# Kernel tuning notes

Hardware: AMD Instinct MI355X
Metric: run time of the kernel (lower is better)

The kernel has to match this reference:

```python
import jax, jax.numpy as jnp
import numpy as np

N_HEADS = 12
EMBED_DIM = 768
QKV_DIM = 64


def setup_inputs() -> dict:
    key = jax.random.key(0)
    ks = jax.random.split(key, 6)
    x = jax.random.normal(ks[0], (32, 577, EMBED_DIM), dtype=jnp.float32)
    # per-head Linear weights, torch layout [out, in] stacked over heads: [H, D, E]
    s = 1.0 / np.sqrt(EMBED_DIM)
    wq = jax.random.uniform(ks[1], (N_HEADS, QKV_DIM, EMBED_DIM), jnp.float32, -s, s)
    wk = jax.random.uniform(ks[2], (N_HEADS, QKV_DIM, EMBED_DIM), jnp.float32, -s, s)
    wv = jax.random.uniform(ks[3], (N_HEADS, QKV_DIM, EMBED_DIM), jnp.float32, -s, s)
    sp = 1.0 / np.sqrt(N_HEADS * QKV_DIM)
    w_proj = jax.random.uniform(ks[4], (EMBED_DIM, N_HEADS * QKV_DIM), jnp.float32, -sp, sp)
    b_proj = jax.random.uniform(ks[5], (EMBED_DIM,), jnp.float32, -sp, sp)
    return {"x": x, "wq": wq, "wk": wk, "wv": wv, "w_proj": w_proj, "b_proj": b_proj}


def reference(x, wq, wk, wv, w_proj, b_proj):
    scale = QKV_DIM ** (-0.5)
    # batched per-head projections: x [B,S,E], w* [H,D,E] -> [B,H,S,D]
    q = jnp.einsum('bse,hde->bhsd', x, wq)
    k = jnp.einsum('bse,hde->bhsd', x, wk)
    v = jnp.einsum('bse,hde->bhsd', x, wv)
    scores = jnp.einsum('bhsd,bhtd->bhst', q, k) * scale  # [B,H,S,S]
    attn = jax.nn.softmax(scores, axis=-1)
    out = jnp.einsum('bhst,bhtd->bhsd', attn, v)          # [B,H,S,D]
    # concat heads in head order along last dim: [B,S,H*D]
    B, H, S, D = out.shape
    cat = jnp.transpose(out, (0, 2, 1, 3)).reshape(B, S, H * D)
    return cat @ w_proj.T + b_proj
```

## Files before the change

kernel.cpp:

```cpp
#include <hip/hip_runtime.h>

#define TOK    18464
#define SEQ    577
#define EMB    768
#define NH     12
#define HD     64
#define HEADSZ 36928
#define PLANE  14180352
#define SPAD   640

typedef float f32x4 __attribute__((ext_vector_type(4)));
typedef short s16x8 __attribute__((ext_vector_type(8)));

__device__ __forceinline__ unsigned short f2bf(float f) {
  unsigned u = __builtin_bit_cast(unsigned, f);
  return (unsigned short)((u + 0x7fffu + ((u >> 16) & 1u)) >> 16);
}
__device__ __forceinline__ unsigned pk2bf(float a, float b) {
  return (unsigned)f2bf(a) | ((unsigned)f2bf(b) << 16);
}
__device__ __forceinline__ float fexp2(float x) {
  float r; asm("v_exp_f32 %0, %1" : "=v"(r) : "v"(x)); return r;
}

__device__ __forceinline__ void gload16(const void* g, void* l) {
  __builtin_amdgcn_global_load_lds(
      (const __attribute__((address_space(1))) void*)g,
      (__attribute__((address_space(3))) void*)l, 16, 0, 0);
}

__global__ void cvt_x(const float* __restrict__ src, short* __restrict__ dst, int n8) {
  int i = blockIdx.x * blockDim.x + threadIdx.x;
  if (i >= n8) return;
  const float4* s4 = reinterpret_cast<const float4*>(src + (size_t)i * 8);
  float4 a = s4[0], b = s4[1];
  s16x8 o;
  o[0] = (short)f2bf(a.x); o[1] = (short)f2bf(a.y);
  o[2] = (short)f2bf(a.z); o[3] = (short)f2bf(a.w);
  o[4] = (short)f2bf(b.x); o[5] = (short)f2bf(b.y);
  o[6] = (short)f2bf(b.z); o[7] = (short)f2bf(b.w);
  *reinterpret_cast<s16x8*>(dst + (size_t)i * 8) = o;
}

__global__ void cvt_w(const float* __restrict__ wq, const float* __restrict__ wk,
                      const float* __restrict__ wv, const float* __restrict__ wp,
                      short* __restrict__ wqkv, short* __restrict__ wpb) {
  int tid = blockIdx.x * blockDim.x + threadIdx.x;
  if (tid >= 294912) return;
  int region = tid / 73728;
  int off = (tid % 73728) * 8;
  const float* s; short* d;
  if (region == 0)      { s = wq + off; d = wqkv + off; }
  else if (region == 1) { s = wk + off; d = wqkv + 589824 + off; }
  else if (region == 2) { s = wv + off; d = wqkv + 2 * 589824 + off; }
  else                  { s = wp + off; d = wpb + off; }
  const float4* s4 = reinterpret_cast<const float4*>(s);
  float4 a = s4[0], b = s4[1];
  s16x8 o;
  o[0] = (short)f2bf(a.x); o[1] = (short)f2bf(a.y);
  o[2] = (short)f2bf(a.z); o[3] = (short)f2bf(a.w);
  o[4] = (short)f2bf(b.x); o[5] = (short)f2bf(b.y);
  o[6] = (short)f2bf(b.z); o[7] = (short)f2bf(b.w);
  *reinterpret_cast<s16x8*>(d) = o;
}

template <int MODE>
__launch_bounds__(512)
__global__ void gemm_bt(const short* __restrict__ A, const short* __restrict__ Bw,
                        short* __restrict__ qk_out, short* __restrict__ vt_out,
                        float* __restrict__ out, const float* __restrict__ bias,
                        int M, int nnt) {
  __shared__ char Asb[32768];
  __shared__ char Bsb[16384];
  int bid = blockIdx.x, nwg = gridDim.x;
  int qq = nwg >> 3, rr = nwg & 7;
  int xcd = bid & 7, loc = bid >> 3;
  int wgid = (xcd < rr ? xcd * (qq + 1) : rr * (qq + 1) + (xcd - rr) * qq) + loc;
  int tn = wgid % nnt;
  int tm = wgid / nnt;
  int tid = threadIdx.x;
  int w = tid >> 6, lane = tid & 63;
  int wm = w >> 1, wn = w & 1;
  int lr = lane & 15, lg = lane >> 4;
  int m0 = tm * 256, n0 = tn * 128;

  f32x4 acc[4][4] = {};

  int srow = tid >> 3;
  int scb  = (tid & 7) * 16;
  int cbs  = scb ^ ((srow & 7) << 4);
  const char* Ab = (const char*)A;
  const char* Bb = (const char*)Bw;
  int swz = (lr & 7) << 4;

  for (int kt = 0; kt < 12; ++kt) {
    size_t kbB = (size_t)kt * 128;
    __syncthreads();
    #pragma unroll
    for (int it = 0; it < 4; ++it) {
      int row = srow + it * 64;
      int gr = m0 + row; if (gr >= M) gr = M - 1;
      gload16(Ab + (size_t)gr * (EMB * 2) + kbB + cbs, Asb + row * 128 + scb);
    }
    #pragma unroll
    for (int it = 0; it < 2; ++it) {
      int row = srow + it * 64;
      int rb = n0 + row;
      gload16(Bb + (size_t)rb * (EMB * 2) + kbB + cbs, Bsb + row * 128 + scb);
    }
    __syncthreads();

    #pragma unroll
    for (int kk = 0; kk < 2; ++kk) {
      int cb = (kk * 64 + lg * 16) ^ swz;
      s16x8 af[4], bfr[4];
      #pragma unroll
      for (int f = 0; f < 4; ++f)
        af[f] = *reinterpret_cast<const s16x8*>(Asb + (wm * 64 + f * 16 + lr) * 128 + cb);
      #pragma unroll
      for (int f = 0; f < 4; ++f)
        bfr[f] = *reinterpret_cast<const s16x8*>(Bsb + (wn * 64 + f * 16 + lr) * 128 + cb);
      #pragma unroll
      for (int i = 0; i < 4; ++i)
        #pragma unroll
        for (int j = 0; j < 4; ++j)
          acc[i][j] = __builtin_amdgcn_mfma_f32_16x16x32_bf16(af[i], bfr[j], acc[i][j], 0, 0, 0);
    }
  }

  int mbase = m0 + wm * 64;
  int nbase = n0 + wn * 64;
  #pragma unroll
  for (int i = 0; i < 4; ++i) {
    #pragma unroll
    for (int j = 0; j < 4; ++j) {
      #pragma unroll
      for (int r = 0; r < 4; ++r) {
        int row = mbase + i * 16 + lg * 4 + r;
        int col = nbase + j * 16 + lr;
        if (row < M) {
          float v = acc[i][j][r];
          if (MODE == 0) {
            int b = row / SEQ;
            int s = row - b * SEQ;
            if (col >= 1536) {
              int rem = col - 1536;
              int h = rem >> 6, d = rem & 63;
              vt_out[((size_t)(b * NH + h) * HD + d) * SPAD + s] = (short)f2bf(v);
            } else {
              int which = (col >= 768) ? 1 : 0;
              int rem = col - which * 768;
              int h = rem >> 6, d = rem & 63;
              qk_out[(size_t)which * PLANE + ((size_t)b * NH + h) * HEADSZ + s * HD + d] =
                  (short)f2bf(v);
            }
          } else {
            out[(size_t)row * EMB + col] = v + bias[col];
          }
        }
      }
    }
  }
}

__launch_bounds__(256)
__global__ void attn(const short* __restrict__ qkv, const short* __restrict__ vt,
                     short* __restrict__ cat) {
  int bid = blockIdx.x;
  int wgid = (bid & 7) * 240 + (bid >> 3);
  int bh = wgid / 5, qt = wgid % 5;
  int b = bh / NH, h = bh % NH;
  const short* Q   = qkv + (size_t)bh * HEADSZ;
  const char* KpB  = (const char*)(qkv + (size_t)PLANE + (size_t)bh * HEADSZ);
  const char* VtpB = (const char*)(vt + (size_t)bh * (HD * SPAD));

  __shared__ char KVs[16384];
  __shared__ short Pl[4][32 * 72];

  int tid = threadIdx.x, w = tid >> 6, lane = tid & 63;
  int lr = lane & 15, lg = lane >> 4;
  int q0 = qt * 128;
  short* Pw = &Pl[w][0];

  s16x8 qf[2][2];
  #pragma unroll
  for (int rb = 0; rb < 2; ++rb) {
    int row = q0 + w * 32 + rb * 16 + lr; if (row >= SEQ) row = SEQ - 1;
    #pragma unroll
    for (int kk = 0; kk < 2; ++kk)
      qf[rb][kk] = *reinterpret_cast<const s16x8*>(&Q[row * HD + kk * 32 + lg * 8]);
  }

  int srow0 = tid >> 3;
  int scb   = (tid & 7) * 16;
  int swz  = (lr & 7) << 4;
  int ka0  = lr * 128 + ((lg * 16) ^ swz);

  f32x4 acco[2][4] = {};
  float lsum[2] = {0.f, 0.f};
  const float SCL = 0.18033688f;
  const f32x4 NEG16 = {-16.f, -16.f, -16.f, -16.f};

  for (int tt = 0; tt < 10; ++tt) {
    int t0 = tt * 64;

    __syncthreads();
    #pragma unroll
    for (int it = 0; it < 2; ++it) {
      int row = srow0 + it * 32;
      int cb  = scb ^ ((row & 7) << 4);
      int ldst = row * 128 + scb;
      int grow = t0 + row; if (grow > 576) grow = 576;
      gload16(KpB + (size_t)grow * 128 + cb, KVs + ldst);
      gload16(VtpB + (size_t)row * (SPAD * 2) + t0 * 2 + cb, KVs + 8192 + ldst);
    }
    __syncthreads();

    #pragma unroll
    for (int fk = 0; fk < 4; ++fk) {
      s16x8 kf0 = *reinterpret_cast<const s16x8*>(KVs + fk * 2048 + ka0);
      s16x8 kf1 = *reinterpret_cast<const s16x8*>(KVs + fk * 2048 + (ka0 ^ 64));
      f32x4 s0 = NEG16, s1 = NEG16;
      s0 = __builtin_amdgcn_mfma_f32_16x16x32_bf16(kf0, qf[0][0], s0, 0, 0, 0);
      s0 = __builtin_amdgcn_mfma_f32_16x16x32_bf16(kf1, qf[0][1], s0, 0, 0, 0);
      s1 = __builtin_amdgcn_mfma_f32_16x16x32_bf16(kf0, qf[1][0], s1, 0, 0, 0);
      s1 = __builtin_amdgcn_mfma_f32_16x16x32_bf16(kf1, qf[1][1], s1, 0, 0, 0);
      #pragma unroll
      for (int r = 0; r < 4; ++r) {
        bool ok = (t0 + fk * 16 + lg * 4 + r) < SEQ;
        s0[r] = ok ? s0[r] * SCL : -1e30f;
        s1[r] = ok ? s1[r] * SCL : -1e30f;
      }
      {
        float p0 = fexp2(s0[0]), p1 = fexp2(s0[1]);
        float p2 = fexp2(s0[2]), p3 = fexp2(s0[3]);
        lsum[0] += (p0 + p1) + (p2 + p3);
        uint2 pk; pk.x = pk2bf(p0, p1); pk.y = pk2bf(p2, p3);
        *reinterpret_cast<uint2*>(&Pw[(size_t)lr * 72 + fk * 16 + lg * 4]) = pk;
      }
      {
        float p0 = fexp2(s1[0]), p1 = fexp2(s1[1]);
        float p2 = fexp2(s1[2]), p3 = fexp2(s1[3]);
        lsum[1] += (p0 + p1) + (p2 + p3);
        uint2 pk; pk.x = pk2bf(p0, p1); pk.y = pk2bf(p2, p3);
        *reinterpret_cast<uint2*>(&Pw[(size_t)(16 + lr) * 72 + fk * 16 + lg * 4]) = pk;
      }
    }

    s16x8 pf[2][2];
    #pragma unroll
    for (int rb = 0; rb < 2; ++rb)
      #pragma unroll
      for (int kk = 0; kk < 2; ++kk)
        pf[rb][kk] = *reinterpret_cast<const s16x8*>(&Pw[(rb * 16 + lr) * 72 + kk * 32 + lg * 8]);

    #pragma unroll
    for (int f = 0; f < 4; ++f) {
      s16x8 vf0 = *reinterpret_cast<const s16x8*>(KVs + 8192 + f * 2048 + ka0);
      s16x8 vf1 = *reinterpret_cast<const s16x8*>(KVs + 8192 + f * 2048 + (ka0 ^ 64));
      acco[0][f] = __builtin_amdgcn_mfma_f32_16x16x32_bf16(pf[0][0], vf0, acco[0][f], 0, 0, 0);
      acco[0][f] = __builtin_amdgcn_mfma_f32_16x16x32_bf16(pf[0][1], vf1, acco[0][f], 0, 0, 0);
      acco[1][f] = __builtin_amdgcn_mfma_f32_16x16x32_bf16(pf[1][0], vf0, acco[1][f], 0, 0, 0);
      acco[1][f] = __builtin_amdgcn_mfma_f32_16x16x32_bf16(pf[1][1], vf1, acco[1][f], 0, 0, 0);
    }
  }

  #pragma unroll
  for (int rb = 0; rb < 2; ++rb) {
    lsum[rb] += __shfl_xor(lsum[rb], 16);
    lsum[rb] += __shfl_xor(lsum[rb], 32);
  }

  #pragma unroll
  for (int rb = 0; rb < 2; ++rb) {
    #pragma unroll
    for (int r = 0; r < 4; ++r) {
      float li = __shfl(lsum[rb], lg * 4 + r);
      int s = q0 + w * 32 + rb * 16 + lg * 4 + r;
      if (s < SEQ) {
        float inv = 1.0f / li;
        #pragma unroll
        for (int f = 0; f < 4; ++f)
          cat[((size_t)b * SEQ + s) * EMB + h * HD + f * 16 + lr] =
              (short)f2bf(acco[rb][f][r] * inv);
      }
    }
  }
}

extern "C" void kernel_launch(void* const* d_in, const int* in_sizes, int n_in,
                              void* d_out, int out_size, void* d_ws, size_t ws_size,
                              hipStream_t stream) {
  const float* x  = (const float*)d_in[0];
  const float* wq = (const float*)d_in[1];
  const float* wk = (const float*)d_in[2];
  const float* wv = (const float*)d_in[3];
  const float* wp = (const float*)d_in[4];
  const float* bp = (const float*)d_in[5];
  float* out = (float*)d_out;

  char* ws = (char*)d_ws;
  short* xb   = (short*)ws;
  short* wqkv = (short*)(ws + 28360704);
  short* wpb  = (short*)(ws + 31899648);
  short* qkb  = (short*)(ws + 33079296);
  short* vtb  = (short*)(ws + 89800704);
  short* cat  = xb;

  hipMemsetAsync(vtb, 0, 31457280, stream);
  cvt_x<<<6924, 256, 0, stream>>>(x, xb, 1772544);
  cvt_w<<<1152, 256, 0, stream>>>(wq, wk, wv, wp, wqkv, wpb);
  gemm_bt<0><<<73 * 18, 512, 0, stream>>>(xb, wqkv, qkb, vtb, nullptr, nullptr, TOK, 18);
  attn<<<1920, 256, 0, stream>>>(qkb, vtb, cat);
  gemm_bt<1><<<73 * 6, 512, 0, stream>>>(cat, wpb, nullptr, nullptr, out, bp, TOK, 6);
}
```

Baseline: 240.9 us.

## Triple-buffer GEMM LDS tiles with interleaved async loads and MFMA phases

Replaces the single-buffered load/sync/compute loop in both projection GEMMs with a three-stage LDS ring in dynamic shared memory. Global-to-LDS loads for tile t+2 are issued in four slices between MFMA phases, and s_waitcnt vmcnt counters stand in for full syncthreads, so memory latency can overlap compute. LDS use rises to 144KB per block, which caps occupancy at one workgroup per CU, and correctness now rests on hand-counted vmcnt values.

```diff
diff --git a/kernel.cpp b/kernel.cpp
--- a/kernel.cpp
+++ b/kernel.cpp
@@ -70,8 +70,7 @@
                         short* __restrict__ qk_out, short* __restrict__ vt_out,
                         float* __restrict__ out, const float* __restrict__ bias,
                         int M, int nnt) {
-  __shared__ char Asb[32768];
-  __shared__ char Bsb[16384];
+  extern __shared__ char lds[];
   int bid = blockIdx.x, nwg = gridDim.x;
   int qq = nwg >> 3, rr = nwg & 7;
   int xcd = bid & 7, loc = bid >> 3;
@@ -93,40 +92,87 @@
   const char* Bb = (const char*)Bw;
   int swz = (lr & 7) << 4;
 
-  for (int kt = 0; kt < 12; ++kt) {
-    size_t kbB = (size_t)kt * 128;
-    __syncthreads();
-    #pragma unroll
-    for (int it = 0; it < 4; ++it) {
-      int row = srow + it * 64;
-      int gr = m0 + row; if (gr >= M) gr = M - 1;
-      gload16(Ab + (size_t)gr * (EMB * 2) + kbB + cbs, Asb + row * 128 + scb);
-    }
-    #pragma unroll
-    for (int it = 0; it < 2; ++it) {
-      int row = srow + it * 64;
-      int rb = n0 + row;
-      gload16(Bb + (size_t)rb * (EMB * 2) + kbB + cbs, Bsb + row * 128 + scb);
-    }
-    __syncthreads();
-
-    #pragma unroll
-    for (int kk = 0; kk < 2; ++kk) {
-      int cb = (kk * 64 + lg * 16) ^ swz;
-      s16x8 af[4], bfr[4];
-      #pragma unroll
-      for (int f = 0; f < 4; ++f)
-        af[f] = *reinterpret_cast<const s16x8*>(Asb + (wm * 64 + f * 16 + lr) * 128 + cb);
-      #pragma unroll
-      for (int f = 0; f < 4; ++f)
-        bfr[f] = *reinterpret_cast<const s16x8*>(Bsb + (wn * 64 + f * 16 + lr) * 128 + cb);
-      #pragma unroll
-      for (int i = 0; i < 4; ++i)
-        #pragma unroll
-        for (int j = 0; j < 4; ++j)
-          acc[i][j] = __builtin_amdgcn_mfma_f32_16x16x32_bf16(af[i], bfr[j], acc[i][j], 0, 0, 0);
-    }
-  }
+#define SA(buf, kB, c)                                                      \
+  { int row = srow + (c) * 64; int gr = m0 + row; if (gr >= M) gr = M - 1;  \
+    gload16(Ab + (size_t)gr * 1536 + (kB) + cbs, (buf) + row * 128 + scb); }
+#define SB(buf, kB, c)                                                      \
+  { int row = srow + (c) * 64; int rb = n0 + row;                           \
+    gload16(Bb + (size_t)rb * 1536 + (kB) + cbs, (buf) + 32768 + row * 128 + scb); }
+
+  SA(lds, 0, 0) SA(lds, 0, 1) SA(lds, 0, 2) SA(lds, 0, 3)
+  SB(lds, 0, 0) SB(lds, 0, 1)
+  SA(lds + 49152, 128, 0) SA(lds + 49152, 128, 1) SA(lds + 49152, 128, 2) SA(lds + 49152, 128, 3)
+  SB(lds + 49152, 128, 0) SB(lds + 49152, 128, 1)
+  asm volatile("s_waitcnt vmcnt(6)" ::: "memory");
+  __builtin_amdgcn_s_barrier();
+
+  for (int t = 0; t < 12; ++t) {
+    const char* Abuf = lds + 49152 * (t % 3);
+    const char* Bbuf = Abuf + 32768;
+    char* sbuf = lds + 49152 * ((t + 2) % 3);
+    size_t kS = (size_t)(t + 2) * 128;
+    bool st = (t < 10);
+
+    s16x8 af0, af1, bfr[4];
+    {
+      int cb = (lg * 16) ^ swz;
+      #pragma unroll
+      for (int nf = 0; nf < 4; ++nf)
+        bfr[nf] = *reinterpret_cast<const s16x8*>(Bbuf + (wn * 64 + nf * 16 + lr) * 128 + cb);
+      af0 = *reinterpret_cast<const s16x8*>(Abuf + (wm * 64 + lr) * 128 + cb);
+      af1 = *reinterpret_cast<const s16x8*>(Abuf + (wm * 64 + 16 + lr) * 128 + cb);
+      if (st) { SA(sbuf, kS, 0) SA(sbuf, kS, 1) }
+      #pragma unroll
+      for (int nf = 0; nf < 4; ++nf) {
+        acc[0][nf] = __builtin_amdgcn_mfma_f32_16x16x32_bf16(af0, bfr[nf], acc[0][nf], 0, 0, 0);
+        acc[1][nf] = __builtin_amdgcn_mfma_f32_16x16x32_bf16(af1, bfr[nf], acc[1][nf], 0, 0, 0);
+      }
+      __builtin_amdgcn_s_barrier();
+    }
+    {
+      int cb = (lg * 16) ^ swz;
+      af0 = *reinterpret_cast<const s16x8*>(Abuf + (wm * 64 + 32 + lr) * 128 + cb);
+      af1 = *reinterpret_cast<const s16x8*>(Abuf + (wm * 64 + 48 + lr) * 128 + cb);
+      if (st) { SA(sbuf, kS, 2) SA(sbuf, kS, 3) }
+      #pragma unroll
+      for (int nf = 0; nf < 4; ++nf) {
+        acc[2][nf] = __builtin_amdgcn_mfma_f32_16x16x32_bf16(af0, bfr[nf], acc[2][nf], 0, 0, 0);
+        acc[3][nf] = __builtin_amdgcn_mfma_f32_16x16x32_bf16(af1, bfr[nf], acc[3][nf], 0, 0, 0);
+      }
+      __builtin_amdgcn_s_barrier();
+    }
+    {
+      int cb = (64 + lg * 16) ^ swz;
+      #pragma unroll
+      for (int nf = 0; nf < 4; ++nf)
+        bfr[nf] = *reinterpret_cast<const s16x8*>(Bbuf + (wn * 64 + nf * 16 + lr) * 128 + cb);
+      af0 = *reinterpret_cast<const s16x8*>(Abuf + (wm * 64 + lr) * 128 + cb);
+      af1 = *reinterpret_cast<const s16x8*>(Abuf + (wm * 64 + 16 + lr) * 128 + cb);
+      if (st) { SB(sbuf, kS, 0) }
+      #pragma unroll
+      for (int nf = 0; nf < 4; ++nf) {
+        acc[0][nf] = __builtin_amdgcn_mfma_f32_16x16x32_bf16(af0, bfr[nf], acc[0][nf], 0, 0, 0);
+        acc[1][nf] = __builtin_amdgcn_mfma_f32_16x16x32_bf16(af1, bfr[nf], acc[1][nf], 0, 0, 0);
+      }
+      __builtin_amdgcn_s_barrier();
+    }
+    {
+      int cb = (64 + lg * 16) ^ swz;
+      af0 = *reinterpret_cast<const s16x8*>(Abuf + (wm * 64 + 32 + lr) * 128 + cb);
+      af1 = *reinterpret_cast<const s16x8*>(Abuf + (wm * 64 + 48 + lr) * 128 + cb);
+      if (st) { SB(sbuf, kS, 1) }
+      #pragma unroll
+      for (int nf = 0; nf < 4; ++nf) {
+        acc[2][nf] = __builtin_amdgcn_mfma_f32_16x16x32_bf16(af0, bfr[nf], acc[2][nf], 0, 0, 0);
+        acc[3][nf] = __builtin_amdgcn_mfma_f32_16x16x32_bf16(af1, bfr[nf], acc[3][nf], 0, 0, 0);
+      }
+      if (t < 10)       { asm volatile("s_waitcnt vmcnt(6)" ::: "memory"); }
+      else if (t == 10) { asm volatile("s_waitcnt vmcnt(0)" ::: "memory"); }
+      if (t < 11) __builtin_amdgcn_s_barrier();
+    }
+  }
+#undef SA
+#undef SB
 
   int mbase = m0 + wm * 64;
   int nbase = n0 + wn * 64;
@@ -310,7 +356,7 @@
   hipMemsetAsync(vtb, 0, 31457280, stream);
   cvt_x<<<6924, 256, 0, stream>>>(x, xb, 1772544);
   cvt_w<<<1152, 256, 0, stream>>>(wq, wk, wv, wp, wqkv, wpb);
-  gemm_bt<0><<<73 * 18, 512, 0, stream>>>(xb, wqkv, qkb, vtb, nullptr, nullptr, TOK, 18);
+  gemm_bt<0><<<73 * 18, 512, 147456, stream>>>(xb, wqkv, qkb, vtb, nullptr, nullptr, TOK, 18);
   attn<<<1920, 256, 0, stream>>>(qkb, vtb, cat);
-  gemm_bt<1><<<73 * 6, 512, 0, stream>>>(cat, wpb, nullptr, nullptr, out, bp, TOK, 6);
-}
+  gemm_bt<1><<<73 * 6, 512, 147456, stream>>>(cat, wpb, nullptr, nullptr, out, bp, TOK, 6);
+}
```

New measurement: 258.0 us. 1.07x slower.
